# Kernel tuning notes

Measured on AMD Instinct MI355X. Metric: run time of the kernel, lower is better.

Reference implementation:

```python
import jax, jax.numpy as jnp
import numpy as np

IN_DIMS = 1024
OUT_DIMS = 1024
N_TOKENS = 32768


def setup_inputs() -> dict:
    key = jax.random.key(0)
    k_x, k_wl0, k_wl1, k_scale, k_shift, k_noise = jax.random.split(key, 6)
    x = jax.random.normal(k_x, (N_TOKENS, IN_DIMS), dtype=jnp.float32)
    # weight_logits[..., 0]: magnitude logits, weight_logits[..., 1]: sign logits
    gain = np.sqrt(2.0)  # relu gain
    a = gain * np.sqrt(6.0 / (IN_DIMS + OUT_DIMS))
    mag_logits = jax.random.uniform(k_wl0, (OUT_DIMS, IN_DIMS), dtype=jnp.float32,
                                    minval=-a, maxval=a)  # logit(0.5)=0, so centered at 0
    sgn_logits = jax.random.uniform(k_wl1, (OUT_DIMS, IN_DIMS), dtype=jnp.float32,
                                    minval=-a, maxval=a)
    weight_logits = jnp.stack([mag_logits, sgn_logits], axis=-1)  # [O, I, 2]
    scale = jnp.full((OUT_DIMS,), np.float32(a), dtype=jnp.float32)
    shift = jnp.full((OUT_DIMS,), 0.01, dtype=jnp.float32)
    noise = jax.random.normal(k_noise, (N_TOKENS, OUT_DIMS), dtype=jnp.float32)
    return {"x": x, "weight_logits": weight_logits, "scale": scale,
            "shift": shift, "noise": noise}


def reference(x, weight_logits, scale, shift, noise):
    # train_forward of TernaryLinear
    weight_p = jax.nn.sigmoid(weight_logits)          # [O, I, 2]
    p_mag = weight_p[..., 0]                          # P(|w| = 1)
    p_sgn = weight_p[..., 1]                          # P(w > 0 | |w| = 1)
    s = 2.0 * p_sgn - 1.0
    weight_mean = p_mag * s                           # [O, I]
    weight_var = p_mag - (p_mag * p_mag) * (s * s)    # [O, I], >= 0
    out_mean = jnp.einsum('ni,oi->no', x, weight_mean)         # [N, O]
    out_var = jnp.einsum('ni,oi->no', x * x, weight_var)       # [N, O]
    out = out_mean + jnp.sqrt(out_var) * noise
    out = out * scale[None, :] + shift[None, :]
    return out
```

## Files before the change

kernel.cpp:

```cpp
#include <hip/hip_runtime.h>
#include <hip/hip_bf16.h>
#include <cmath>

#define N_TOK 32768
#define KDIM  1024
#define ODIM  1024

#define BM 128
#define BN 128
#define BK 64
#define NKT (KDIM / BK)
#define THREADS 512

typedef float          f32x4  __attribute__((ext_vector_type(4)));
typedef __bf16         bf16x8 __attribute__((ext_vector_type(8)));
typedef unsigned short us8    __attribute__((ext_vector_type(8)));
typedef unsigned short us2    __attribute__((ext_vector_type(2)));

static __device__ __forceinline__ unsigned short f2bf(float f) {
  unsigned u = __builtin_bit_cast(unsigned, f);
  u += 0x7FFFu + ((u >> 16) & 1u);
  return (unsigned short)(u >> 16);
}
static __device__ __forceinline__ unsigned short bfc(float f) {
  return __builtin_bit_cast(unsigned short, (__bf16)f);
}
static __device__ __forceinline__ float bf2f(unsigned short u) {
  return __builtin_bit_cast(float, (unsigned)u << 16);
}

static __device__ __forceinline__ f32x4 mfma16(us8 a, us8 b, f32x4 c) {
  return __builtin_amdgcn_mfma_f32_16x16x32_bf16(
      __builtin_bit_cast(bf16x8, a), __builtin_bit_cast(bf16x8, b), c, 0, 0, 0);
}

static __device__ __forceinline__ void gl_lds16(const void* g, void* l) {
  __builtin_amdgcn_global_load_lds(
      (const __attribute__((address_space(1))) void*)g,
      (__attribute__((address_space(3))) void*)l, 16, 0, 0);
}

static __device__ __forceinline__ us8 sqr8(us8 a) {
  us8 r;
#pragma unroll
  for (int i = 0; i < 8; ++i) {
    float f = bf2f(a[i]);
    r[i] = bfc(f * f);
  }
  return r;
}

__global__ void wprep_kernel(const float* __restrict__ wl,
                             unsigned short* __restrict__ wm,
                             unsigned short* __restrict__ wv) {
  int i = blockIdx.x * blockDim.x + threadIdx.x;
  f32x4 v = *reinterpret_cast<const f32x4*>(wl + (size_t)i * 4);
  float pm0 = 1.f / (1.f + expf(-v.x));
  float ps0 = 1.f / (1.f + expf(-v.y));
  float pm1 = 1.f / (1.f + expf(-v.z));
  float ps1 = 1.f / (1.f + expf(-v.w));
  float m0 = pm0 * (2.f * ps0 - 1.f);
  float m1 = pm1 * (2.f * ps1 - 1.f);
  float q0 = pm0 - m0 * m0;
  float q1 = pm1 - m1 * m1;
  us2 am = {f2bf(m0), f2bf(m1)};
  us2 av = {f2bf(q0), f2bf(q1)};
  *reinterpret_cast<us2*>(wm + (size_t)i * 2) = am;
  *reinterpret_cast<us2*>(wv + (size_t)i * 2) = av;
}

__global__ void xprep_kernel(const float* __restrict__ x,
                             unsigned short* __restrict__ xbf) {
  const int t = blockIdx.x * blockDim.x + threadIdx.x;
#pragma unroll
  for (int i = 0; i < 4; ++i) {
    size_t c = (size_t)i * 1048576 + t;
    const float* s = x + c * 8;
    f32x4 v0 = *reinterpret_cast<const f32x4*>(s);
    f32x4 v1 = *reinterpret_cast<const f32x4*>(s + 4);
    us8 o = {bfc(v0.x), bfc(v0.y), bfc(v0.z), bfc(v0.w),
             bfc(v1.x), bfc(v1.y), bfc(v1.z), bfc(v1.w)};
    *reinterpret_cast<us8*>(xbf + c * 8) = o;
  }
}

template <bool PRE>
__global__ __launch_bounds__(THREADS, 2) void ternary_gemm(
    const float* __restrict__ x,
    const unsigned short* __restrict__ xbf,
    const unsigned short* __restrict__ wm,
    const unsigned short* __restrict__ wv,
    const float* __restrict__ scale,
    const float* __restrict__ shift,
    const float* __restrict__ noise,
    float* __restrict__ out) {
  __shared__ alignas(16) char smem[49152];

  const int tid  = threadIdx.x;
  const int lane = tid & 63;
  const int w    = tid >> 6;
  const bool isVar = (w >= 4);
  const int p    = w & 3;
  const int wr   = p >> 1;
  const int wc   = p & 1;
  const int l15  = lane & 15;
  const int l4   = lane >> 4;

  const int bid = blockIdx.x;
  const int swz = (bid & 7) * 256 + (bid >> 3);
  const int bm  = swz >> 3;
  const int bn  = swz & 7;
  const int rowBase = bm * BM;
  const int colBase = bn * BN;

  f32x4 acc[4][4];
#pragma unroll
  for (int i = 0; i < 4; ++i)
#pragma unroll
    for (int j = 0; j < 4; ++j) acc[i][j] = (f32x4)0.f;

  for (int kt = 0; kt < NKT; ++kt) {
    const int k0 = kt * BK;

#pragma unroll
    for (int c = 0; c < 2; ++c) {
      int flat = c * THREADS + tid;
      int row  = flat >> 3;
      int j    = flat & 7;
      size_t go = (size_t)(colBase + row) * KDIM + k0 + ((j ^ (row & 7)) << 3);
      gl_lds16(wm + go, smem + 16384 + flat * 16);
      gl_lds16(wv + go, smem + 32768 + flat * 16);
    }
    if constexpr (PRE) {
#pragma unroll
      for (int c = 0; c < 2; ++c) {
        int flat = c * THREADS + tid;
        int row  = flat >> 3;
        int j    = flat & 7;
        size_t go = (size_t)(rowBase + row) * KDIM + k0 + ((j ^ (row & 7)) << 3);
        gl_lds16(xbf + go, smem + flat * 16);
      }
    } else {
#pragma unroll
      for (int c = 0; c < 2; ++c) {
        int flat = c * THREADS + tid;
        int row  = flat >> 3;
        int j    = flat & 7;
        const float* s = x + (size_t)(rowBase + row) * KDIM + k0 + j * 8;
        f32x4 v0 = *reinterpret_cast<const f32x4*>(s);
        f32x4 v1 = *reinterpret_cast<const f32x4*>(s + 4);
        us8 o = {bfc(v0.x), bfc(v0.y), bfc(v0.z), bfc(v0.w),
                 bfc(v1.x), bfc(v1.y), bfc(v1.z), bfc(v1.w)};
        int off = row * 128 + ((j * 16) ^ ((row & 7) << 4));
        *reinterpret_cast<us8*>(smem + off) = o;
      }
    }
    __syncthreads();

    const char* Bb = smem + 16384 + (isVar ? 16384 : 0);
#pragma unroll
    for (int ks = 0; ks < 2; ++ks) {
      const int kb = ks * 64 + (l4 << 4);
      us8 bfr[4], afr[4];
#pragma unroll
      for (int b = 0; b < 4; ++b) {
        int row = wc * 64 + b * 16 + l15;
        bfr[b] = *reinterpret_cast<const us8*>(Bb + row * 128 + (kb ^ ((row & 7) << 4)));
      }
#pragma unroll
      for (int a = 0; a < 4; ++a) {
        int row = wr * 64 + a * 16 + l15;
        afr[a] = *reinterpret_cast<const us8*>(smem + row * 128 + (kb ^ ((row & 7) << 4)));
        if (isVar) afr[a] = sqr8(afr[a]);
      }
      __builtin_amdgcn_s_setprio(1);
#pragma unroll
      for (int a = 0; a < 4; ++a)
#pragma unroll
        for (int b = 0; b < 4; ++b)
          acc[a][b] = mfma16(afr[a], bfr[b], acc[a][b]);
      __builtin_amdgcn_s_setprio(0);
    }
    __syncthreads();
  }

  unsigned short* MxB = (unsigned short*)smem;
  unsigned short* VxB = (unsigned short*)(smem + 16384);
  if (!isVar) {
#pragma unroll
    for (int i = 2; i < 4; ++i)
#pragma unroll
      for (int b = 0; b < 4; ++b)
#pragma unroll
        for (int j = 0; j < 4; ++j) {
          int lr = (i - 2) * 16 + l4 * 4 + j;
          int lc = b * 16 + l15;
          MxB[(p * 32 + lr) * 64 + (lc ^ (((lr >> 2) & 3) << 4))] = bfc(acc[i][b][j]);
        }
  } else {
#pragma unroll
    for (int i = 0; i < 2; ++i)
#pragma unroll
      for (int b = 0; b < 4; ++b)
#pragma unroll
        for (int j = 0; j < 4; ++j) {
          int lr = i * 16 + l4 * 4 + j;
          int lc = b * 16 + l15;
          VxB[(p * 32 + lr) * 64 + (lc ^ (((lr >> 2) & 3) << 4))] = bfc(acc[i][b][j]);
        }
  }
  __syncthreads();

  if (!isVar) {
#pragma unroll
    for (int i = 0; i < 2; ++i)
#pragma unroll
      for (int b = 0; b < 4; ++b) {
        int col = colBase + wc * 64 + b * 16 + l15;
        float sc = scale[col], sh = shift[col];
#pragma unroll
        for (int j = 0; j < 4; ++j) {
          int lr = i * 16 + l4 * 4 + j;
          int lc = b * 16 + l15;
          float vv = bf2f(VxB[(p * 32 + lr) * 64 + (lc ^ (((lr >> 2) & 3) << 4))]);
          size_t idx = (size_t)(rowBase + wr * 64 + lr) * ODIM + col;
          out[idx] = fmaf(acc[i][b][j] + sqrtf(fmaxf(vv, 0.f)) * noise[idx], sc, sh);
        }
      }
  } else {
#pragma unroll
    for (int i = 2; i < 4; ++i)
#pragma unroll
      for (int b = 0; b < 4; ++b) {
        int col = colBase + wc * 64 + b * 16 + l15;
        float sc = scale[col], sh = shift[col];
#pragma unroll
        for (int j = 0; j < 4; ++j) {
          int lr = (i - 2) * 16 + l4 * 4 + j;
          int lc = b * 16 + l15;
          float mm = bf2f(MxB[(p * 32 + lr) * 64 + (lc ^ (((lr >> 2) & 3) << 4))]);
          size_t idx = (size_t)(rowBase + wr * 64 + 32 + lr) * ODIM + col;
          out[idx] = fmaf(mm + sqrtf(fmaxf(acc[i][b][j], 0.f)) * noise[idx], sc, sh);
        }
      }
  }
}

extern "C" void kernel_launch(void* const* d_in, const int* in_sizes, int n_in,
                              void* d_out, int out_size, void* d_ws, size_t ws_size,
                              hipStream_t stream) {
  const float* x     = (const float*)d_in[0];
  const float* wl    = (const float*)d_in[1];
  const float* scale = (const float*)d_in[2];
  const float* shift = (const float*)d_in[3];
  const float* noise = (const float*)d_in[4];
  float* out = (float*)d_out;

  unsigned short* wm  = (unsigned short*)d_ws;
  unsigned short* wv  = wm + (size_t)ODIM * KDIM;
  unsigned short* xbf = wv + (size_t)ODIM * KDIM;

  const size_t need = 2ull * ODIM * KDIM * 2 + (size_t)N_TOK * KDIM * 2;
  const bool pre = (ws_size >= need);

  wprep_kernel<<<(ODIM * KDIM / 2) / 256, 256, 0, stream>>>(wl, wm, wv);
  if (pre)
    xprep_kernel<<<4096, 256, 0, stream>>>(x, xbf);

  if (pre)
    ternary_gemm<true><<<2048, THREADS, 0, stream>>>(
        x, xbf, wm, wv, scale, shift, noise, out);
  else
    ternary_gemm<false><<<2048, THREADS, 0, stream>>>(
        x, xbf, wm, wv, scale, shift, noise, out);
}
```

Baseline: 233.2 us.

## Double-buffer LDS tiles with BK=32 and raise occupancy target

Halves the K tile to 32 and adds a two-buffer LDS ring, so the loads for tile kt+1 are issued while tile kt is fed to MFMA. This leaves one barrier per K step instead of two, aiming to hide global-to-LDS latency behind compute. The launch bounds change from 2 to 4 blocks per CU. That caps the register budget well below the 64 fp32 accumulators each thread holds, so spilling is likely, and four 48KB LDS blocks may not fit on a CU anyway. The halved K step also doubles the number of loop iterations and barriers.

```diff
diff --git a/kernel.cpp b/kernel.cpp
--- a/kernel.cpp
+++ b/kernel.cpp
@@ -8,9 +8,10 @@
 
 #define BM 128
 #define BN 128
-#define BK 64
+#define BK 32
 #define NKT (KDIM / BK)
 #define THREADS 512
+#define BUFSZ 24576
 
 typedef float          f32x4  __attribute__((ext_vector_type(4)));
 typedef __bf16         bf16x8 __attribute__((ext_vector_type(8)));
@@ -84,8 +85,8 @@
   }
 }
 
-template <bool PRE>
-__global__ __launch_bounds__(THREADS, 2) void ternary_gemm(
+template <int PRE>
+__global__ __launch_bounds__(THREADS, 4) void ternary_gemm(
     const float* __restrict__ x,
     const unsigned short* __restrict__ xbf,
     const unsigned short* __restrict__ wm,
@@ -94,7 +95,7 @@
     const float* __restrict__ shift,
     const float* __restrict__ noise,
     float* __restrict__ out) {
-  __shared__ alignas(16) char smem[49152];
+  __shared__ alignas(16) char smem[2 * BUFSZ];
 
   const int tid  = threadIdx.x;
   const int lane = tid & 63;
@@ -119,68 +120,59 @@
 #pragma unroll
     for (int j = 0; j < 4; ++j) acc[i][j] = (f32x4)0.f;
 
+  const int srow = tid >> 2;
+  const int sj   = tid & 3;
+  const int ke   = (sj ^ (srow & 3)) << 3;
+  const size_t gB = (size_t)(colBase + srow) * KDIM + ke;
+  const size_t gA = (size_t)(rowBase + srow) * KDIM + ke;
+
+  auto stage = [&](int kt, char* buf) {
+    const int k0 = kt * BK;
+    gl_lds16(wm + gB + k0, buf + 8192 + tid * 16);
+    gl_lds16(wv + gB + k0, buf + 16384 + tid * 16);
+    if constexpr (PRE) {
+      gl_lds16(xbf + gA + k0, buf + tid * 16);
+    } else {
+      const float* s = x + gA + k0;
+      f32x4 v0 = *reinterpret_cast<const f32x4*>(s);
+      f32x4 v1 = *reinterpret_cast<const f32x4*>(s + 4);
+      us8 o = {bfc(v0.x), bfc(v0.y), bfc(v0.z), bfc(v0.w),
+               bfc(v1.x), bfc(v1.y), bfc(v1.z), bfc(v1.w)};
+      int off = srow * 64 + ((sj * 16) ^ ((srow & 3) << 4));
+      *reinterpret_cast<us8*>(buf + off) = o;
+    }
+  };
+
+  stage(0, smem);
+  __syncthreads();
+
   for (int kt = 0; kt < NKT; ++kt) {
-    const int k0 = kt * BK;
-
-#pragma unroll
-    for (int c = 0; c < 2; ++c) {
-      int flat = c * THREADS + tid;
-      int row  = flat >> 3;
-      int j    = flat & 7;
-      size_t go = (size_t)(colBase + row) * KDIM + k0 + ((j ^ (row & 7)) << 3);
-      gl_lds16(wm + go, smem + 16384 + flat * 16);
-      gl_lds16(wv + go, smem + 32768 + flat * 16);
+    const char* cur = smem + (size_t)(kt & 1) * BUFSZ;
+    if (kt + 1 < NKT)
+      stage(kt + 1, smem + (size_t)((kt + 1) & 1) * BUFSZ);
+
+    const char* Bb = cur + 8192 + (isVar ? 8192 : 0);
+    const int kb = l4 << 4;
+    us8 bfr[4], afr[4];
+#pragma unroll
+    for (int b = 0; b < 4; ++b) {
+      int row = wc * 64 + b * 16 + l15;
+      bfr[b] = *reinterpret_cast<const us8*>(Bb + row * 64 + (kb ^ ((row & 3) << 4)));
     }
-    if constexpr (PRE) {
-#pragma unroll
-      for (int c = 0; c < 2; ++c) {
-        int flat = c * THREADS + tid;
-        int row  = flat >> 3;
-        int j    = flat & 7;
-        size_t go = (size_t)(rowBase + row) * KDIM + k0 + ((j ^ (row & 7)) << 3);
-        gl_lds16(xbf + go, smem + flat * 16);
-      }
-    } else {
-#pragma unroll
-      for (int c = 0; c < 2; ++c) {
-        int flat = c * THREADS + tid;
-        int row  = flat >> 3;
-        int j    = flat & 7;
-        const float* s = x + (size_t)(rowBase + row) * KDIM + k0 + j * 8;
-        f32x4 v0 = *reinterpret_cast<const f32x4*>(s);
-        f32x4 v1 = *reinterpret_cast<const f32x4*>(s + 4);
-        us8 o = {bfc(v0.x), bfc(v0.y), bfc(v0.z), bfc(v0.w),
-                 bfc(v1.x), bfc(v1.y), bfc(v1.z), bfc(v1.w)};
-        int off = row * 128 + ((j * 16) ^ ((row & 7) << 4));
-        *reinterpret_cast<us8*>(smem + off) = o;
-      }
+#pragma unroll
+    for (int a = 0; a < 4; ++a) {
+      int row = wr * 64 + a * 16 + l15;
+      afr[a] = *reinterpret_cast<const us8*>(cur + row * 64 + (kb ^ ((row & 3) << 4)));
+      if (isVar) afr[a] = sqr8(afr[a]);
     }
-    __syncthreads();
-
-    const char* Bb = smem + 16384 + (isVar ? 16384 : 0);
-#pragma unroll
-    for (int ks = 0; ks < 2; ++ks) {
-      const int kb = ks * 64 + (l4 << 4);
-      us8 bfr[4], afr[4];
-#pragma unroll
-      for (int b = 0; b < 4; ++b) {
-        int row = wc * 64 + b * 16 + l15;
-        bfr[b] = *reinterpret_cast<const us8*>(Bb + row * 128 + (kb ^ ((row & 7) << 4)));
-      }
-#pragma unroll
-      for (int a = 0; a < 4; ++a) {
-        int row = wr * 64 + a * 16 + l15;
-        afr[a] = *reinterpret_cast<const us8*>(smem + row * 128 + (kb ^ ((row & 7) << 4)));
-        if (isVar) afr[a] = sqr8(afr[a]);
-      }
-      __builtin_amdgcn_s_setprio(1);
-#pragma unroll
-      for (int a = 0; a < 4; ++a)
-#pragma unroll
-        for (int b = 0; b < 4; ++b)
-          acc[a][b] = mfma16(afr[a], bfr[b], acc[a][b]);
-      __builtin_amdgcn_s_setprio(0);
-    }
+    __builtin_amdgcn_s_setprio(1);
+#pragma unroll
+    for (int a = 0; a < 4; ++a)
+#pragma unroll
+      for (int b = 0; b < 4; ++b)
+        acc[a][b] = mfma16(afr[a], bfr[b], acc[a][b]);
+    __builtin_amdgcn_s_setprio(0);
+
     __syncthreads();
   }
 
@@ -268,9 +260,9 @@
     xprep_kernel<<<4096, 256, 0, stream>>>(x, xbf);
 
   if (pre)
-    ternary_gemm<true><<<2048, THREADS, 0, stream>>>(
+    ternary_gemm<1><<<2048, THREADS, 0, stream>>>(
         x, xbf, wm, wv, scale, shift, noise, out);
   else
-    ternary_gemm<false><<<2048, THREADS, 0, stream>>>(
+    ternary_gemm<0><<<2048, THREADS, 0, stream>>>(
         x, xbf, wm, wv, scale, shift, noise, out);
 }
```

New measurement: 240.3 us. 3.0% more time.
